# Kernel optimization log

Measured on AMD Instinct MI355X. Metric: run time of the kernel, lower is better.

Reference implementation:

```python
import jax, jax.numpy as jnp
import numpy as np

SCALE = 100.0
ALPHA_MEM = 0.9
ALPHA_MEM_OUT = 0.9
ALPHA_R = 0.85
ALPHA_X = 0.95
ALPHA_P = 0.95
ALPHA_D = 0.95
WMIN = 0.0
WMAX = 2.0


@jax.custom_vjp
def spike_fn(x):
    # SurrGradSpike.forward: heaviside(x)
    return (x > 0).astype(x.dtype)

def _spike_fwd(x):
    return spike_fn(x), x

def _spike_bwd(x, g):
    # SurrGradSpike.backward: g / (scale*|x| + 1)^2
    return (g / (SCALE * jnp.abs(x) + 1.0) ** 2,)

spike_fn.defvjp(_spike_fwd, _spike_bwd)


def setup_inputs() -> dict:
    key = jax.random.key(0)
    ks = jax.random.split(key, 8)
    B, T, NI, N, NO, D = 8, 64, 256, 512, 32, 4
    inputs = jax.random.normal(ks[0], (B, T, NI), jnp.float32)
    w = jax.random.normal(ks[1], (N, N), jnp.float32) * (0.1 / np.sqrt(N))
    w_in = jax.random.normal(ks[2], (NI, N), jnp.float32) * (1.0 / np.sqrt(NI))
    w_out = jax.random.normal(ks[3], (N, NO), jnp.float32) * (1.0 / np.sqrt(N))
    # each synapse (e,o) assigned exactly one delay bin -> one-hot delay map (D,N,N)
    delay_idx = jax.random.randint(ks[4], (N, N), 0, D)
    dmap = jax.nn.one_hot(delay_idx, D, axis=0, dtype=jnp.float32)
    delays = jnp.array([1, 2, 3, 5], jnp.int32)
    w_signs = jnp.where(jnp.arange(N) < (4 * N) // 5, 1.0, -1.0).astype(jnp.float32)
    p = jax.random.uniform(ks[5], (N,), jnp.float32, minval=-0.5, maxval=0.5)
    A_p = jax.random.uniform(ks[6], (N, N), jnp.float32, minval=0.0, maxval=1e-3)
    A_d = jax.random.uniform(ks[7], (N, N), jnp.float32, minval=0.0, maxval=1e-3)
    return dict(inputs=inputs, w=w, w_in=w_in, w_out=w_out, dmap=dmap,
                delays=delays, w_signs=w_signs, p=p, A_p=A_p, A_d=A_d)


def _snn_forward(inputs, w, w_in, w_out, dmap, delays, w_signs, p, A_p, A_d):
    B, T, _ = inputs.shape
    N = w.shape[0]
    dt = inputs.dtype
    # epoch state
    inp = jnp.einsum('btc,cn->btn', inputs, w_in)          # (B,T,N)
    W = dmap * (w_signs[:, None] * jnp.abs(w))             # (D,N,N)
    p_depr = (p < 0).astype(dt)

    mem = jnp.zeros((B, N), dt)
    w_p = jnp.zeros((B, N), dt)
    x_bar = jnp.zeros((B, N), dt)
    u_pot = jnp.zeros((B, N), dt)
    u_dep = jnp.zeros((B, N), dt)
    w_stdp = jnp.ones((B, N, N), dt)
    rec_out = jnp.zeros((T, B, N), dt)
    rec_wp = jnp.zeros((T, B, N), dt)
    rec_xb = jnp.zeros((T, B, N), dt)

    def step(carry, xt):
        mem, w_p, x_bar, u_pot, u_dep, w_stdp, rec_out, rec_wp, rec_xb = carry
        t, inp_t = xt
        # mark_spikes + record_state (records pre-update values)
        spike = spike_fn(mem - 1.0)
        rec_out = rec_out.at[t].set(spike)
        rec_wp = rec_wp.at[t].set(w_p)
        rec_xb = rec_xb.at[t].set(x_bar)
        # delayed gathers; negative torch indices hit zero-initialized tail -> %T
        idx = (t - delays) % T
        out_del = jnp.take(rec_out, idx, axis=0)           # (D,B,N)
        wp_del = jnp.take(rec_wp, idx, axis=0)
        xb_del = jnp.take(rec_xb, idx, axis=0)
        # synaptic input
        syn_p = out_del * (1.0 + wp_del)
        syn = jnp.einsum('dbe,deo,beo->bo', syn_p, W, w_stdp)
        # STP
        dw_p = spike * p * (1.0 + p_depr * w_p)
        w_p = w_p * ALPHA_R + dw_p
        # STDP (uses pre-update u_dep/u_pot/mem)
        X = jnp.einsum('dbe,deo->beo', out_del, dmap)
        dW_dep = X * A_d[None] * jax.nn.relu(u_dep)[:, None, :]
        xbar_d = jnp.einsum('dbe,deo->beo', xb_del, dmap)
        dW_pot = xbar_d * A_p[None] * (jax.lax.stop_gradient(spike) * jax.nn.relu(u_pot))[:, None, :]
        x_bar = ALPHA_X * x_bar + (1.0 - ALPHA_X) * jax.lax.stop_gradient(spike)
        u_pot = ALPHA_P * u_pot + (1.0 - ALPHA_P) * mem
        u_dep = ALPHA_D * u_dep + (1.0 - ALPHA_D) * mem
        w_stdp = jnp.clip(w_stdp + dW_pot - dW_dep, WMIN, WMAX)
        # membrane integration with spike reset (detached)
        mem = ALPHA_MEM * mem + inp_t + syn - jax.lax.stop_gradient(spike)
        return (mem, w_p, x_bar, u_pot, u_dep, w_stdp, rec_out, rec_wp, rec_xb), None

    carry = (mem, w_p, x_bar, u_pot, u_dep, w_stdp, rec_out, rec_wp, rec_xb)
    xs = (jnp.arange(T), jnp.swapaxes(inp, 0, 1))
    carry, _ = jax.lax.scan(jax.checkpoint(step), carry, xs)
    rec_out = carry[6]                                     # (T,B,N)
    # readout: leaky integrator over projected spikes
    h2 = jnp.einsum('btn,no->bto', jnp.swapaxes(rec_out, 0, 1), w_out)

    def ro_step(o, h):
        o = ALPHA_MEM_OUT * o + h
        return o, o

    _, readout = jax.lax.scan(ro_step, jnp.zeros((B, h2.shape[-1]), dt),
                              jnp.swapaxes(h2, 0, 1))
    return jnp.swapaxes(readout, 0, 1)                     # (B,T,n_outputs)


def reference(inputs, w, w_in, w_out, dmap, delays, w_signs, p, A_p, A_d):
    return _snn_forward(inputs, w, w_in, w_out, dmap, delays, w_signs, p, A_p, A_d)
```

## Files before the change

### kernel.cpp

```cpp
#include <hip/hip_runtime.h>
#include <stdint.h>


#define B  8
#define T  64
#define NI 256
#define NN 512
#define NO 32
#define DD 4

#define NBLK 256
#define TPB  512
#define OPB  16
#define EGR  32
#define SPL  16
#define EPAD 516

#define REC_ELEMS (T*B*NN)
#define MAGIC  0x534E4E31u

#define C_CNT   0
#define C_GCNT  8
#define C_PAR   9
#define C_HDR   10
#define C_DONE  16

__device__ __forceinline__ unsigned long long rec_load(const unsigned long long* p) {
    return __hip_atomic_load(p, __ATOMIC_RELAXED, __HIP_MEMORY_SCOPE_AGENT);
}
__device__ __forceinline__ unsigned long long rec_load_plain(const unsigned long long* p) {
    return *p;
}
__device__ __forceinline__ void rec_store(unsigned long long* p, unsigned long long v) {
    __hip_atomic_store(p, v, __ATOMIC_RELAXED, __HIP_MEMORY_SCOPE_AGENT);
}
__device__ __forceinline__ unsigned ctrl_ld(const unsigned* p) {
    return __hip_atomic_load(p, __ATOMIC_RELAXED, __HIP_MEMORY_SCOPE_AGENT);
}
__device__ __forceinline__ void ctrl_st(unsigned* p, unsigned v) {
    __hip_atomic_store(p, v, __ATOMIC_RELAXED, __HIP_MEMORY_SCOPE_AGENT);
}
__device__ __forceinline__ bool unwritten(unsigned long long v, unsigned runpar) {
    return ((unsigned)v >> 31) != runpar;
}
__device__ __forceinline__ unsigned long long poll_written(
        const unsigned long long* src, unsigned long long v, unsigned runpar) {
    int guard = 0;
    while (unwritten(v, runpar)) {
        if (guard >= 2) __builtin_amdgcn_s_sleep(1);
        v = rec_load(src);
        if (++guard > (1 << 18)) break;
    }
    return v;
}

#define BAR_LDS() do {                                      \
    asm volatile("s_waitcnt lgkmcnt(0)" ::: "memory");      \
    __builtin_amdgcn_s_barrier();                           \
    asm volatile("" ::: "memory");                          \
} while (0)

__global__ __launch_bounds__(TPB, 2)
void snn_main(const float* __restrict__ inputs,
              const float* __restrict__ w,
              const float* __restrict__ w_in,
              const float* __restrict__ w_out,
              const float* __restrict__ dmap,
              const int*   __restrict__ delays,
              const float* __restrict__ w_signs,
              const float* __restrict__ p,
              const float* __restrict__ A_p,
              const float* __restrict__ A_d,
              unsigned long long* __restrict__ rec,
              float* __restrict__ h2buf,
              unsigned* __restrict__ ctrl,
              float* __restrict__ out)
{
    __shared__ float2 sxq[DD*EPAD];
    __shared__ float  inp_s[T*OPB];
    __shared__ float  red[8*OPB];
    __shared__ unsigned int spikebits_s[T];
    __shared__ float  wout16_s[OPB*NO];
    __shared__ float  h2_s[T*NO];
    __shared__ int    last_s;

    const int tid     = threadIdx.x;
    const int bid     = blockIdx.x;
    const int b       = bid & 7;
    const int chunk   = bid >> 3;
    const int o_base  = chunk * OPB;
    const int o_local = tid & 15;
    const int e_grp   = tid >> 4;
    const int o       = o_base + o_local;

    unsigned runpar;
    if (ctrl_ld(ctrl + C_HDR) != MAGIC) {
        {
            unsigned long long* base = rec + (size_t)bid * (REC_ELEMS / NBLK);
            #pragma unroll
            for (int i = 0; i < REC_ELEMS / NBLK / TPB; ++i)
                rec_store(base + i*TPB + tid, 0x0000000080000000ull);
        }
        {
            unsigned* hb = (unsigned*)h2buf + (size_t)bid * ((B*T*NO) / NBLK);
            if (tid < (B*T*NO) / NBLK) ctrl_st(hb + tid, 0u);
        }
        if (bid == 0 && tid < 10) ctrl_st(ctrl + tid, 0u);
        __syncthreads();
        if (tid == 0) ctrl_st(ctrl + C_DONE + bid, MAGIC);
        if (tid < NBLK) {
            int guard = 0;
            while (ctrl_ld(ctrl + C_DONE + tid) != MAGIC) {
                __builtin_amdgcn_s_sleep(2);
                if (++guard > (1 << 20)) break;
            }
        }
        __syncthreads();
        runpar = 0u;
    } else {
        runpar = ctrl_ld(ctrl + C_PAR);
    }

    if (tid < OPB) {
        rec_store(rec + (size_t)(0*B + b)*NN + o_base + tid,
                  (unsigned long long)(runpar << 31));
    }
    if (tid == 0) spikebits_s[0] = 0u;

    float wv[SPL], ap[SPL], ad[SPL], ws[SPL];
    int   laddr[SPL];
    #pragma unroll
    for (int i = 0; i < SPL; ++i) {
        const int e = e_grp + EGR*i;
        wv[i] = w_signs[e] * fabsf(w[e*NN + o]);
        ap[i] = A_p[e*NN + o];
        ad[i] = A_d[e*NN + o];
        int d = 0;
        if (dmap[1*NN*NN + e*NN + o] != 0.0f) d = 1;
        if (dmap[2*NN*NN + e*NN + o] != 0.0f) d = 2;
        if (dmap[3*NN*NN + e*NN + o] != 0.0f) d = 3;
        ws[i]    = 1.0f;
        laddr[i] = (d*EPAD + e) * 8;
    }
    int del[DD];
    #pragma unroll
    for (int d = 0; d < DD; ++d) del[d] = delays[d];

    {
        float* win = (float*)sxq;
        #pragma unroll
        for (int q = 0; q < NI*OPB/TPB; ++q) {
            const int k = q*TPB + tid;
            const int c = k >> 4, oo = k & 15;
            win[c*OPB + oo] = w_in[c*NN + o_base + oo];
        }
        __syncthreads();
        #pragma unroll
        for (int j = 0; j < T/EGR; ++j) {
            const int tj = e_grp*(T/EGR) + j;
            const float* inrow = inputs + (size_t)(b*T + tj)*NI;
            float a = 0.f;
            for (int c = 0; c < NI; ++c) a += inrow[c] * win[c*OPB + o_local];
            inp_s[tj*OPB + o_local] = a;
        }
        __syncthreads();
    }

    #pragma unroll
    for (int d = 0; d < DD; ++d)
        sxq[d*EPAD + tid] = make_float2(0.f, 0.f);
    __syncthreads();

    float mem = 0.f, w_p = 0.f, x_bar = 0.f, u_pot = 0.f, u_dep = 0.f;
    const float p_o  = p[o];
    const float pd_o = (p_o < 0.f) ? 1.f : 0.f;

    unsigned long long pf[DD];
    const int stage_ord[DD] = {1, 2, 3, 0};

    for (int t = 0; t < T; ++t) {
        if (t + 1 < T) {
            #pragma unroll
            for (int d = 0; d < DD; ++d) {
                if (t + 1 >= del[d]) {
                    const int s = (t + 1 - del[d]) & 63;
                    const unsigned long long* src = rec + (size_t)(s*B + b)*NN + tid;
                    pf[d] = (del[d] == 1) ? rec_load(src) : rec_load_plain(src);
                }
            }
        }

        const float spike = (mem > 1.0f) ? 1.0f : 0.0f;
        const float pg  = spike * fmaxf(u_pot, 0.f);
        const float udr = fmaxf(u_dep, 0.f);
        float2 v[SPL];
        float acc = 0.f;
        #pragma unroll
        for (int i = 0; i < SPL; ++i) {
            v[i] = *(const float2*)((const char*)sxq + laddr[i]);
            acc = fmaf(v[i].x, wv[i]*ws[i], acc);
        }
        float a2 = acc + __shfl_xor(acc, 16);
        a2 += __shfl_xor(a2, 32);
        if ((tid & 63) < 16) red[(tid >> 6)*16 + o_local] = a2;
        BAR_LDS();
        float syn = 0.f;
        #pragma unroll
        for (int k = 0; k < 8; ++k) syn += red[k*16 + o_local];

        const float wp_new = 0.85f*w_p + spike * p_o * (1.f + pd_o*w_p);
        const float xb_new = 0.95f*x_bar + 0.05f*spike;
        u_pot = 0.95f*u_pot + 0.05f*mem;
        u_dep = 0.95f*u_dep + 0.05f*mem;
        mem   = 0.9f*mem + inp_s[t*OPB + o_local] + syn - spike;
        w_p   = wp_new;
        x_bar = xb_new;

        if (t + 1 < T && tid < OPB) {
            const float spike1 = (mem > 1.0f) ? 1.0f : 0.0f;
            const float sp = spike1 * (1.f + w_p);
            const unsigned int xu = __float_as_uint(x_bar) | (spike1 != 0.f ? 0x80000000u : 0u);
            const unsigned int lo = __float_as_uint(sp) | (runpar << 31);
            const unsigned long long pk = ((unsigned long long)xu << 32) | lo;
            rec_store(rec + (size_t)((t+1)*B + b)*NN + o_base + tid, pk);
            const unsigned long long bal = __ballot(spike1 != 0.0f);
            if (tid == 0) spikebits_s[t+1] = (unsigned int)bal;
        }

        #pragma unroll
        for (int i = 0; i < SPL; ++i) {
            const unsigned int xu = __float_as_uint(v[i].y);
            const float dep = ((int)xu < 0) ? ad[i]*udr : 0.f;
            const float pot = (ap[i]*pg) * fabsf(v[i].y);
            ws[i] = fminf(fmaxf(ws[i] + pot - dep, 0.f), 2.f);
        }

        if (t + 1 < T) {
            #pragma unroll
            for (int j = 0; j < DD; ++j) {
                const int d = stage_ord[j];
                unsigned long long v0 = (unsigned long long)(runpar << 31);
                if (t + 1 >= del[d]) {
                    const int s = (t + 1 - del[d]) & 63;
                    const unsigned long long* src = rec + (size_t)(s*B + b)*NN + tid;
                    v0 = poll_written(src, pf[d], runpar);
                }
                sxq[d*EPAD + tid] =
                    make_float2(__uint_as_float((unsigned)v0 & 0x7fffffffu),
                                __uint_as_float((unsigned)(v0 >> 32)));
            }
        }
        BAR_LDS();
    }

    if (tid < OPB*NO) wout16_s[tid] = w_out[(o_base + (tid >> 5))*NO + (tid & 31)];
    __syncthreads();

    const int g  = tid >> 5;
    const int oo = tid & 31;
    #pragma unroll
    for (int j = 0; j < 4; ++j) {
        const int t = g*4 + j;
        const unsigned int bits = spikebits_s[t];
        float a = 0.f;
        #pragma unroll
        for (int i = 0; i < OPB; ++i)
            if (bits & (1u << i)) a += wout16_s[i*NO + oo];
        if (a != 0.f) atomicAdd(h2buf + ((size_t)b*T + t)*NO + oo, a);
    }
    __threadfence();
    __syncthreads();
    if (tid == 0) last_s = (atomicAdd(ctrl + C_CNT + b, 1u) == 31u) ? 1 : 0;
    __syncthreads();

    if (last_s) {
        __threadfence();
        #pragma unroll
        for (int j = 0; j < 4; ++j) {
            const int t = g*4 + j;
            h2_s[t*NO + oo] = __hip_atomic_load(h2buf + ((size_t)b*T + t)*NO + oo,
                                                __ATOMIC_RELAXED, __HIP_MEMORY_SCOPE_AGENT);
        }
        __syncthreads();
        if (tid < NO) {
            float st = 0.f;
            for (int t = 0; t < T; ++t) {
                st = 0.9f*st + h2_s[t*NO + tid];
                out[((size_t)b*T + t)*NO + tid] = st;
            }
        }
    }

    if (tid == 0) {
        const unsigned gar = __hip_atomic_fetch_add(ctrl + C_GCNT, 1u,
                                                    __ATOMIC_ACQ_REL, __HIP_MEMORY_SCOPE_AGENT);
        if (gar == NBLK - 1) {
            for (int i = 0; i < 8; ++i) ctrl_st(ctrl + C_CNT + i, 0u);
            ctrl_st(ctrl + C_GCNT, 0u);
            ctrl_st(ctrl + C_PAR, runpar ^ 1u);
            ctrl_st(ctrl + C_HDR, MAGIC);
        }
    }
}

extern "C" void kernel_launch(void* const* d_in, const int* in_sizes, int n_in,
                              void* d_out, int out_size, void* d_ws, size_t ws_size,
                              hipStream_t stream)
{
    const float* inputs  = (const float*)d_in[0];
    const float* w       = (const float*)d_in[1];
    const float* w_in    = (const float*)d_in[2];
    const float* w_out   = (const float*)d_in[3];
    const float* dmap    = (const float*)d_in[4];
    const int*   delays  = (const int*)  d_in[5];
    const float* w_signs = (const float*)d_in[6];
    const float* p       = (const float*)d_in[7];
    const float* A_p     = (const float*)d_in[8];
    const float* A_d     = (const float*)d_in[9];

    char* wsb = (char*)d_ws;
    unsigned long long* rec = (unsigned long long*)wsb;
    float* h2buf = (float*)(wsb + (size_t)REC_ELEMS*8);
    unsigned* ctrl = (unsigned*)(wsb + (size_t)REC_ELEMS*8 + (size_t)B*T*NO*4);

    hipLaunchKernelGGL(snn_main, dim3(NBLK), dim3(TPB), 0, stream,
                       inputs, w, w_in, w_out, dmap, delays, w_signs, p, A_p, A_d,
                       rec, h2buf, ctrl, (float*)d_out);
}
```

Before: 223.3 us.

## Double-buffer delay staging with 1024 threads per block to halve per-step barriers

Block size grows from 512 to 1024 threads, so each thread handles 8 presynaptic rows instead of 16. The two thread halves each stage two of the four delay buffers. Staging of the next step's spike records now goes into a second LDS buffer and overlaps the current step's matvec, so one barrier per timestep is removed. This also changes initialisation indexing and zeroes h2buf in the last block. It risks higher register pressure and a larger cross-half reduction, and the cooperative spin-wait now depends on more resident threads.

```diff
diff --git a/kernel.cpp b/kernel.cpp
--- a/kernel.cpp
+++ b/kernel.cpp
@@ -10,10 +10,10 @@
 #define DD 4
 
 #define NBLK 256
-#define TPB  512
+#define TPB  1024
 #define OPB  16
-#define EGR  32
-#define SPL  16
+#define EGR  64
+#define SPL  8
 #define EPAD 516
 
 #define REC_ELEMS (T*B*NN)
@@ -60,7 +60,7 @@
     asm volatile("" ::: "memory");                          \
 } while (0)
 
-__global__ __launch_bounds__(TPB, 2)
+__global__ __launch_bounds__(TPB, 4)
 void snn_main(const float* __restrict__ inputs,
               const float* __restrict__ w,
               const float* __restrict__ w_in,
@@ -76,9 +76,9 @@
               unsigned* __restrict__ ctrl,
               float* __restrict__ out)
 {
-    __shared__ float2 sxq[DD*EPAD];
+    __shared__ float2 sxq[2][DD*EPAD];
     __shared__ float  inp_s[T*OPB];
-    __shared__ float  red[8*OPB];
+    __shared__ float  red[2][16*OPB];
     __shared__ unsigned int spikebits_s[T];
     __shared__ float  wout16_s[OPB*NO];
     __shared__ float  h2_s[T*NO];
@@ -92,19 +92,15 @@
     const int o_local = tid & 15;
     const int e_grp   = tid >> 4;
     const int o       = o_base + o_local;
+    const int slotid  = tid & 511;
+    const int hi      = tid >> 9;
 
     unsigned runpar;
     if (ctrl_ld(ctrl + C_HDR) != MAGIC) {
-        {
-            unsigned long long* base = rec + (size_t)bid * (REC_ELEMS / NBLK);
-            #pragma unroll
-            for (int i = 0; i < REC_ELEMS / NBLK / TPB; ++i)
-                rec_store(base + i*TPB + tid, 0x0000000080000000ull);
-        }
-        {
-            unsigned* hb = (unsigned*)h2buf + (size_t)bid * ((B*T*NO) / NBLK);
-            if (tid < (B*T*NO) / NBLK) ctrl_st(hb + tid, 0u);
-        }
+        rec_store(rec + (size_t)bid * (REC_ELEMS / NBLK) + tid,
+                  0x0000000080000000ull);
+        if (tid < (B*T*NO) / NBLK)
+            ctrl_st((unsigned*)h2buf + (size_t)bid * ((B*T*NO) / NBLK) + tid, 0u);
         if (bid == 0 && tid < 10) ctrl_st(ctrl + tid, 0u);
         __syncthreads();
         if (tid == 0) ctrl_st(ctrl + C_DONE + bid, MAGIC);
@@ -145,6 +141,8 @@
     int del[DD];
     #pragma unroll
     for (int d = 0; d < DD; ++d) del[d] = delays[d];
+    const int dj0 = hi ? 2 : 1;
+    const int dj1 = hi ? 0 : 3;
 
     {
         float* win = (float*)sxq;
@@ -155,38 +153,42 @@
             win[c*OPB + oo] = w_in[c*NN + o_base + oo];
         }
         __syncthreads();
-        #pragma unroll
-        for (int j = 0; j < T/EGR; ++j) {
-            const int tj = e_grp*(T/EGR) + j;
+        {
+            const int tj = tid >> 4;
             const float* inrow = inputs + (size_t)(b*T + tj)*NI;
             float a = 0.f;
             for (int c = 0; c < NI; ++c) a += inrow[c] * win[c*OPB + o_local];
+            __syncthreads();
             inp_s[tj*OPB + o_local] = a;
         }
-        __syncthreads();
-    }
-
-    #pragma unroll
-    for (int d = 0; d < DD; ++d)
-        sxq[d*EPAD + tid] = make_float2(0.f, 0.f);
+    }
+
+    if (tid < 512) {
+        #pragma unroll
+        for (int d = 0; d < DD; ++d)
+            sxq[0][d*EPAD + tid] = make_float2(0.f, 0.f);
+    }
     __syncthreads();
 
     float mem = 0.f, w_p = 0.f, x_bar = 0.f, u_pot = 0.f, u_dep = 0.f;
     const float p_o  = p[o];
     const float pd_o = (p_o < 0.f) ? 1.f : 0.f;
 
-    unsigned long long pf[DD];
-    const int stage_ord[DD] = {1, 2, 3, 0};
-
     for (int t = 0; t < T; ++t) {
+        const int cur = t & 1, nxt = cur ^ 1;
+        const char* sxc = (const char*)&sxq[cur][0];
+
+        unsigned long long pf0 = 0ull, pf1 = 0ull;
         if (t + 1 < T) {
-            #pragma unroll
-            for (int d = 0; d < DD; ++d) {
-                if (t + 1 >= del[d]) {
-                    const int s = (t + 1 - del[d]) & 63;
-                    const unsigned long long* src = rec + (size_t)(s*B + b)*NN + tid;
-                    pf[d] = (del[d] == 1) ? rec_load(src) : rec_load_plain(src);
-                }
+            if (t + 1 >= del[dj0]) {
+                const int s = (t + 1 - del[dj0]) & 63;
+                const unsigned long long* src = rec + (size_t)(s*B + b)*NN + slotid;
+                pf0 = (del[dj0] == 1) ? rec_load(src) : rec_load_plain(src);
+            }
+            if (t + 1 >= del[dj1]) {
+                const int s = (t + 1 - del[dj1]) & 63;
+                const unsigned long long* src = rec + (size_t)(s*B + b)*NN + slotid;
+                pf1 = (del[dj1] == 1) ? rec_load(src) : rec_load_plain(src);
             }
         }
 
@@ -197,16 +199,41 @@
         float acc = 0.f;
         #pragma unroll
         for (int i = 0; i < SPL; ++i) {
-            v[i] = *(const float2*)((const char*)sxq + laddr[i]);
+            v[i] = *(const float2*)(sxc + laddr[i]);
             acc = fmaf(v[i].x, wv[i]*ws[i], acc);
         }
         float a2 = acc + __shfl_xor(acc, 16);
         a2 += __shfl_xor(a2, 32);
-        if ((tid & 63) < 16) red[(tid >> 6)*16 + o_local] = a2;
+        if ((tid & 63) < 16) red[cur][(tid >> 6)*16 + o_local] = a2;
+
+        if (t + 1 < T) {
+            {
+                unsigned long long v0 = (unsigned long long)(runpar << 31);
+                if (t + 1 >= del[dj0]) {
+                    const int s = (t + 1 - del[dj0]) & 63;
+                    v0 = poll_written(rec + (size_t)(s*B + b)*NN + slotid, pf0, runpar);
+                }
+                sxq[nxt][dj0*EPAD + slotid] =
+                    make_float2(__uint_as_float((unsigned)v0 & 0x7fffffffu),
+                                __uint_as_float((unsigned)(v0 >> 32)));
+            }
+            {
+                unsigned long long v1 = (unsigned long long)(runpar << 31);
+                if (t + 1 >= del[dj1]) {
+                    const int s = (t + 1 - del[dj1]) & 63;
+                    v1 = poll_written(rec + (size_t)(s*B + b)*NN + slotid, pf1, runpar);
+                }
+                sxq[nxt][dj1*EPAD + slotid] =
+                    make_float2(__uint_as_float((unsigned)v1 & 0x7fffffffu),
+                                __uint_as_float((unsigned)(v1 >> 32)));
+            }
+        }
+
         BAR_LDS();
+
         float syn = 0.f;
         #pragma unroll
-        for (int k = 0; k < 8; ++k) syn += red[k*16 + o_local];
+        for (int k = 0; k < 16; ++k) syn += red[cur][k*16 + o_local];
 
         const float wp_new = 0.85f*w_p + spike * p_o * (1.f + pd_o*w_p);
         const float xb_new = 0.95f*x_bar + 0.05f*spike;
@@ -234,33 +261,17 @@
             const float pot = (ap[i]*pg) * fabsf(v[i].y);
             ws[i] = fminf(fmaxf(ws[i] + pot - dep, 0.f), 2.f);
         }
-
-        if (t + 1 < T) {
-            #pragma unroll
-            for (int j = 0; j < DD; ++j) {
-                const int d = stage_ord[j];
-                unsigned long long v0 = (unsigned long long)(runpar << 31);
-                if (t + 1 >= del[d]) {
-                    const int s = (t + 1 - del[d]) & 63;
-                    const unsigned long long* src = rec + (size_t)(s*B + b)*NN + tid;
-                    v0 = poll_written(src, pf[d], runpar);
-                }
-                sxq[d*EPAD + tid] =
-                    make_float2(__uint_as_float((unsigned)v0 & 0x7fffffffu),
-                                __uint_as_float((unsigned)(v0 >> 32)));
-            }
-        }
-        BAR_LDS();
-    }
-
+    }
+
+    __syncthreads();
     if (tid < OPB*NO) wout16_s[tid] = w_out[(o_base + (tid >> 5))*NO + (tid & 31)];
     __syncthreads();
 
     const int g  = tid >> 5;
     const int oo = tid & 31;
     #pragma unroll
-    for (int j = 0; j < 4; ++j) {
-        const int t = g*4 + j;
+    for (int j = 0; j < 2; ++j) {
+        const int t = g*2 + j;
         const unsigned int bits = spikebits_s[t];
         float a = 0.f;
         #pragma unroll
@@ -276,12 +287,18 @@
     if (last_s) {
         __threadfence();
         #pragma unroll
-        for (int j = 0; j < 4; ++j) {
-            const int t = g*4 + j;
+        for (int j = 0; j < 2; ++j) {
+            const int t = g*2 + j;
             h2_s[t*NO + oo] = __hip_atomic_load(h2buf + ((size_t)b*T + t)*NO + oo,
                                                 __ATOMIC_RELAXED, __HIP_MEMORY_SCOPE_AGENT);
         }
         __syncthreads();
+        #pragma unroll
+        for (int j = 0; j < 2; ++j) {
+            const int t = g*2 + j;
+            __hip_atomic_store((unsigned*)(h2buf + ((size_t)b*T + t)*NO + oo), 0u,
+                               __ATOMIC_RELAXED, __HIP_MEMORY_SCOPE_AGENT);
+        }
         if (tid < NO) {
             float st = 0.f;
             for (int t = 0; t < T; ++t) {
```

Measured after the change: 249.1 us. 11.5% more time.

## Load delayed spikes directly from global per synapse, drop LDS staging barrier

Applied to the files above, without the earlier changes.

Replaces the per-step LDS staging of delayed presynaptic state (with polling and a second block barrier) by having each thread prefetch its 16 synapse values straight from the global recurrence buffer, indexed by a precomputed per-synapse delay offset. Values for the next step are double-buffered in registers and only polled if the parity bit shows they are unwritten, and the reduction buffer is double-buffered so one barrier per step suffices. This removes a barrier and LDS traffic per timestep, at the cost of 16 uncoalesced global atomic loads per thread per step instead of 4 coalesced ones. It also reuses shared scratch and zeroes h2buf in the last block so the next call starts clean.

```diff
diff --git a/kernel.cpp b/kernel.cpp
--- a/kernel.cpp
+++ b/kernel.cpp
@@ -14,8 +14,8 @@
 #define OPB  16
 #define EGR  32
 #define SPL  16
-#define EPAD 516
-
+
+#define RECB (B*NN*8)
 #define REC_ELEMS (T*B*NN)
 #define MAGIC  0x534E4E31u
 
@@ -28,9 +28,6 @@
 __device__ __forceinline__ unsigned long long rec_load(const unsigned long long* p) {
     return __hip_atomic_load(p, __ATOMIC_RELAXED, __HIP_MEMORY_SCOPE_AGENT);
 }
-__device__ __forceinline__ unsigned long long rec_load_plain(const unsigned long long* p) {
-    return *p;
-}
 __device__ __forceinline__ void rec_store(unsigned long long* p, unsigned long long v) {
     __hip_atomic_store(p, v, __ATOMIC_RELAXED, __HIP_MEMORY_SCOPE_AGENT);
 }
@@ -42,16 +39,6 @@
 }
 __device__ __forceinline__ bool unwritten(unsigned long long v, unsigned runpar) {
     return ((unsigned)v >> 31) != runpar;
-}
-__device__ __forceinline__ unsigned long long poll_written(
-        const unsigned long long* src, unsigned long long v, unsigned runpar) {
-    int guard = 0;
-    while (unwritten(v, runpar)) {
-        if (guard >= 2) __builtin_amdgcn_s_sleep(1);
-        v = rec_load(src);
-        if (++guard > (1 << 18)) break;
-    }
-    return v;
 }
 
 #define BAR_LDS() do {                                      \
@@ -76,12 +63,10 @@
               unsigned* __restrict__ ctrl,
               float* __restrict__ out)
 {
-    __shared__ float2 sxq[DD*EPAD];
+    __shared__ float scratch[NI*OPB];
     __shared__ float  inp_s[T*OPB];
-    __shared__ float  red[8*OPB];
+    __shared__ float  red[2][8*OPB];
     __shared__ unsigned int spikebits_s[T];
-    __shared__ float  wout16_s[OPB*NO];
-    __shared__ float  h2_s[T*NO];
     __shared__ int    last_s;
 
     const int tid     = threadIdx.x;
@@ -101,10 +86,8 @@
             for (int i = 0; i < REC_ELEMS / NBLK / TPB; ++i)
                 rec_store(base + i*TPB + tid, 0x0000000080000000ull);
         }
-        {
-            unsigned* hb = (unsigned*)h2buf + (size_t)bid * ((B*T*NO) / NBLK);
-            if (tid < (B*T*NO) / NBLK) ctrl_st(hb + tid, 0u);
-        }
+        if (tid < (B*T*NO) / NBLK)
+            ctrl_st((unsigned*)h2buf + (size_t)bid * ((B*T*NO) / NBLK) + tid, 0u);
         if (bid == 0 && tid < 10) ctrl_st(ctrl + tid, 0u);
         __syncthreads();
         if (tid == 0) ctrl_st(ctrl + C_DONE + bid, MAGIC);
@@ -128,7 +111,8 @@
     if (tid == 0) spikebits_s[0] = 0u;
 
     float wv[SPL], ap[SPL], ad[SPL], ws[SPL];
-    int   laddr[SPL];
+    int   voff[SPL];
+    unsigned long long dpk = 0ull;
     #pragma unroll
     for (int i = 0; i < SPL; ++i) {
         const int e = e_grp + EGR*i;
@@ -139,18 +123,15 @@
         if (dmap[1*NN*NN + e*NN + o] != 0.0f) d = 1;
         if (dmap[2*NN*NN + e*NN + o] != 0.0f) d = 2;
         if (dmap[3*NN*NN + e*NN + o] != 0.0f) d = 3;
-        ws[i]    = 1.0f;
-        laddr[i] = (d*EPAD + e) * 8;
-    }
-    int del[DD];
-    #pragma unroll
-    for (int d = 0; d < DD; ++d) del[d] = delays[d];
+        const int dly = delays[d];
+        ws[i]   = 1.0f;
+        dpk    |= (unsigned long long)(unsigned)dly << (4*i);
+        voff[i] = (b*NN + e)*8 - dly*RECB;
+    }
 
     {
-        float* win = (float*)sxq;
-        #pragma unroll
-        for (int q = 0; q < NI*OPB/TPB; ++q) {
-            const int k = q*TPB + tid;
+        float* win = scratch;
+        for (int k = tid; k < NI*OPB; k += TPB) {
             const int c = k >> 4, oo = k & 15;
             win[c*OPB + oo] = w_in[c*NN + o_base + oo];
         }
@@ -166,26 +147,39 @@
         __syncthreads();
     }
 
-    #pragma unroll
-    for (int d = 0; d < DD; ++d)
-        sxq[d*EPAD + tid] = make_float2(0.f, 0.f);
-    __syncthreads();
-
     float mem = 0.f, w_p = 0.f, x_bar = 0.f, u_pot = 0.f, u_dep = 0.f;
     const float p_o  = p[o];
     const float pd_o = (p_o < 0.f) ? 1.f : 0.f;
 
-    unsigned long long pf[DD];
-    const int stage_ord[DD] = {1, 2, 3, 0};
-
-    for (int t = 0; t < T; ++t) {
+    const float tz = __uint_as_float(runpar << 31);
+    float2 vA[SPL], vB[SPL];
+    #pragma unroll
+    for (int i = 0; i < SPL; ++i) vA[i] = make_float2(tz, 0.f);
+
+    auto STEP = [&](int t, float2 (&vc)[SPL], float2 (&vn)[SPL]) {
+        const char* base1 = (const char*)rec + (size_t)(t+1)*RECB;
+
         if (t + 1 < T) {
-            #pragma unroll
-            for (int d = 0; d < DD; ++d) {
-                if (t + 1 >= del[d]) {
-                    const int s = (t + 1 - del[d]) & 63;
-                    const unsigned long long* src = rec + (size_t)(s*B + b)*NN + tid;
-                    pf[d] = (del[d] == 1) ? rec_load(src) : rec_load_plain(src);
+            if (t >= 4) {
+                #pragma unroll
+                for (int i = 0; i < SPL; ++i) {
+                    const unsigned long long v =
+                        rec_load((const unsigned long long*)(base1 + (long)voff[i]));
+                    vn[i] = make_float2(__uint_as_float((unsigned)v),
+                                        __uint_as_float((unsigned)(v >> 32)));
+                }
+            } else {
+                #pragma unroll
+                for (int i = 0; i < SPL; ++i) {
+                    const int dly = (int)((dpk >> (4*i)) & 15ull);
+                    float2 r = make_float2(tz, 0.f);
+                    if (t + 1 >= dly) {
+                        const unsigned long long v =
+                            rec_load((const unsigned long long*)(base1 + (long)voff[i]));
+                        r = make_float2(__uint_as_float((unsigned)v),
+                                        __uint_as_float((unsigned)(v >> 32)));
+                    }
+                    vn[i] = r;
                 }
             }
         }
@@ -193,20 +187,33 @@
         const float spike = (mem > 1.0f) ? 1.0f : 0.0f;
         const float pg  = spike * fmaxf(u_pot, 0.f);
         const float udr = fmaxf(u_dep, 0.f);
-        float2 v[SPL];
         float acc = 0.f;
         #pragma unroll
         for (int i = 0; i < SPL; ++i) {
-            v[i] = *(const float2*)((const char*)sxq + laddr[i]);
-            acc = fmaf(v[i].x, wv[i]*ws[i], acc);
-        }
+            unsigned lo = __float_as_uint(vc[i].x);
+            if (__builtin_expect((lo >> 31) != runpar, 0)) {
+                const unsigned long long* srcf = (const unsigned long long*)
+                    ((const char*)rec + (size_t)t*RECB + (long)voff[i]);
+                unsigned long long v; int guard = 0;
+                do {
+                    v = rec_load(srcf);
+                    if (++guard > 2) __builtin_amdgcn_s_sleep(1);
+                    if (guard > (1 << 18)) break;
+                } while (unwritten(v, runpar));
+                lo = (unsigned)v;
+                vc[i].y = __uint_as_float((unsigned)(v >> 32));
+            }
+            const float x = __uint_as_float(lo & 0x7fffffffu);
+            acc = fmaf(x, wv[i]*ws[i], acc);
+        }
+
         float a2 = acc + __shfl_xor(acc, 16);
         a2 += __shfl_xor(a2, 32);
-        if ((tid & 63) < 16) red[(tid >> 6)*16 + o_local] = a2;
+        if ((tid & 63) < 16) red[t & 1][(tid >> 6)*16 + o_local] = a2;
         BAR_LDS();
         float syn = 0.f;
         #pragma unroll
-        for (int k = 0; k < 8; ++k) syn += red[k*16 + o_local];
+        for (int k = 0; k < 8; ++k) syn += red[t & 1][k*16 + o_local];
 
         const float wp_new = 0.85f*w_p + spike * p_o * (1.f + pd_o*w_p);
         const float xb_new = 0.95f*x_bar + 0.05f*spike;
@@ -229,31 +236,23 @@
 
         #pragma unroll
         for (int i = 0; i < SPL; ++i) {
-            const unsigned int xu = __float_as_uint(v[i].y);
+            const unsigned int xu = __float_as_uint(vc[i].y);
             const float dep = ((int)xu < 0) ? ad[i]*udr : 0.f;
-            const float pot = (ap[i]*pg) * fabsf(v[i].y);
+            const float pot = (ap[i]*pg) * fabsf(vc[i].y);
             ws[i] = fminf(fmaxf(ws[i] + pot - dep, 0.f), 2.f);
         }
-
-        if (t + 1 < T) {
-            #pragma unroll
-            for (int j = 0; j < DD; ++j) {
-                const int d = stage_ord[j];
-                unsigned long long v0 = (unsigned long long)(runpar << 31);
-                if (t + 1 >= del[d]) {
-                    const int s = (t + 1 - del[d]) & 63;
-                    const unsigned long long* src = rec + (size_t)(s*B + b)*NN + tid;
-                    v0 = poll_written(src, pf[d], runpar);
-                }
-                sxq[d*EPAD + tid] =
-                    make_float2(__uint_as_float((unsigned)v0 & 0x7fffffffu),
-                                __uint_as_float((unsigned)(v0 >> 32)));
-            }
-        }
-        BAR_LDS();
-    }
-
-    if (tid < OPB*NO) wout16_s[tid] = w_out[(o_base + (tid >> 5))*NO + (tid & 31)];
+    };
+
+    for (int t = 0; t < T; t += 2) {
+        STEP(t,     vA, vB);
+        STEP(t + 1, vB, vA);
+    }
+
+    __syncthreads();
+    float* wout16_s = scratch;
+    float* h2_s     = scratch + OPB*NO;
+    for (int k = tid; k < OPB*NO; k += TPB)
+        wout16_s[k] = w_out[(o_base + (k >> 5))*NO + (k & 31)];
     __syncthreads();
 
     const int g  = tid >> 5;
@@ -282,6 +281,12 @@
                                                 __ATOMIC_RELAXED, __HIP_MEMORY_SCOPE_AGENT);
         }
         __syncthreads();
+        #pragma unroll
+        for (int j = 0; j < 4; ++j) {
+            const int t = g*4 + j;
+            __hip_atomic_store((unsigned*)(h2buf + ((size_t)b*T + t)*NO + oo), 0u,
+                               __ATOMIC_RELAXED, __HIP_MEMORY_SCOPE_AGENT);
+        }
         if (tid < NO) {
             float st = 0.f;
             for (int t = 0; t < T; ++t) {
```

Result: slower. 412.7 us (+84.8%).

## Use half as many blocks with 32 outputs each and fuse STDP update

Applied to the files above, without the earlier changes.

Each block now handles 32 output neurons instead of 16, so the persistent grid drops from 256 to 128 blocks and each thread processes 32 presynaptic synapses. The input projection is staged in two halves of w_in so it fits in the shared buffer. The per-synapse STDP weight update is folded into the synaptic accumulation loop, which removes the float2 register array and one shuffle stage. The aim is to cut the number of blocks taking part in the per-timestep cross-block handoff and the polling traffic that goes with it. The cost is a longer serial inner loop per thread and more registers for the per-synapse state.

```diff
diff --git a/kernel.cpp b/kernel.cpp
--- a/kernel.cpp
+++ b/kernel.cpp
@@ -9,11 +9,11 @@
 #define NO 32
 #define DD 4
 
-#define NBLK 256
+#define NBLK 128
 #define TPB  512
-#define OPB  16
-#define EGR  32
-#define SPL  16
+#define OPB  32
+#define EGR  16
+#define SPL  32
 #define EPAD 516
 
 #define REC_ELEMS (T*B*NN)
@@ -80,7 +80,7 @@
     __shared__ float  inp_s[T*OPB];
     __shared__ float  red[8*OPB];
     __shared__ unsigned int spikebits_s[T];
-    __shared__ float  wout16_s[OPB*NO];
+    __shared__ float  wout_s[OPB*NO];
     __shared__ float  h2_s[T*NO];
     __shared__ int    last_s;
 
@@ -89,8 +89,8 @@
     const int b       = bid & 7;
     const int chunk   = bid >> 3;
     const int o_base  = chunk * OPB;
-    const int o_local = tid & 15;
-    const int e_grp   = tid >> 4;
+    const int o_local = tid & 31;
+    const int e_grp   = tid >> 5;
     const int o       = o_base + o_local;
 
     unsigned runpar;
@@ -148,21 +148,32 @@
 
     {
         float* win = (float*)sxq;
-        #pragma unroll
-        for (int q = 0; q < NI*OPB/TPB; ++q) {
-            const int k = q*TPB + tid;
-            const int c = k >> 4, oo = k & 15;
-            win[c*OPB + oo] = w_in[c*NN + o_base + oo];
-        }
-        __syncthreads();
-        #pragma unroll
-        for (int j = 0; j < T/EGR; ++j) {
-            const int tj = e_grp*(T/EGR) + j;
-            const float* inrow = inputs + (size_t)(b*T + tj)*NI;
-            float a = 0.f;
-            for (int c = 0; c < NI; ++c) a += inrow[c] * win[c*OPB + o_local];
-            inp_s[tj*OPB + o_local] = a;
-        }
+        float a[T/EGR];
+        #pragma unroll
+        for (int j = 0; j < T/EGR; ++j) a[j] = 0.f;
+        #pragma unroll
+        for (int half = 0; half < 2; ++half) {
+            const int c0 = half * (NI/2);
+            #pragma unroll
+            for (int q = 0; q < (NI/2)*OPB/TPB; ++q) {
+                const int k = q*TPB + tid;
+                const int c = k >> 5, oo = k & 31;
+                win[c*OPB + oo] = w_in[(c0 + c)*NN + o_base + oo];
+            }
+            __syncthreads();
+            #pragma unroll
+            for (int j = 0; j < T/EGR; ++j) {
+                const int tj = e_grp*(T/EGR) + j;
+                const float* inrow = inputs + (size_t)(b*T + tj)*NI + c0;
+                float s = 0.f;
+                for (int c = 0; c < NI/2; ++c) s += inrow[c] * win[c*OPB + o_local];
+                a[j] += s;
+            }
+            __syncthreads();
+        }
+        #pragma unroll
+        for (int j = 0; j < T/EGR; ++j)
+            inp_s[(e_grp*(T/EGR) + j)*OPB + o_local] = a[j];
         __syncthreads();
     }
 
@@ -193,20 +204,22 @@
         const float spike = (mem > 1.0f) ? 1.0f : 0.0f;
         const float pg  = spike * fmaxf(u_pot, 0.f);
         const float udr = fmaxf(u_dep, 0.f);
-        float2 v[SPL];
         float acc = 0.f;
         #pragma unroll
         for (int i = 0; i < SPL; ++i) {
-            v[i] = *(const float2*)((const char*)sxq + laddr[i]);
-            acc = fmaf(v[i].x, wv[i]*ws[i], acc);
-        }
-        float a2 = acc + __shfl_xor(acc, 16);
-        a2 += __shfl_xor(a2, 32);
-        if ((tid & 63) < 16) red[(tid >> 6)*16 + o_local] = a2;
+            const float2 v = *(const float2*)((const char*)sxq + laddr[i]);
+            acc = fmaf(v.x, wv[i]*ws[i], acc);
+            const unsigned int xu = __float_as_uint(v.y);
+            const float dep = ((int)xu < 0) ? ad[i]*udr : 0.f;
+            const float pot = (ap[i]*pg) * fabsf(v.y);
+            ws[i] = fminf(fmaxf(ws[i] + pot - dep, 0.f), 2.f);
+        }
+        const float a2 = acc + __shfl_xor(acc, 32);
+        if ((tid & 63) < 32) red[(tid >> 6)*32 + o_local] = a2;
         BAR_LDS();
         float syn = 0.f;
         #pragma unroll
-        for (int k = 0; k < 8; ++k) syn += red[k*16 + o_local];
+        for (int k = 0; k < 8; ++k) syn += red[k*32 + o_local];
 
         const float wp_new = 0.85f*w_p + spike * p_o * (1.f + pd_o*w_p);
         const float xb_new = 0.95f*x_bar + 0.05f*spike;
@@ -225,14 +238,6 @@
             rec_store(rec + (size_t)((t+1)*B + b)*NN + o_base + tid, pk);
             const unsigned long long bal = __ballot(spike1 != 0.0f);
             if (tid == 0) spikebits_s[t+1] = (unsigned int)bal;
-        }
-
-        #pragma unroll
-        for (int i = 0; i < SPL; ++i) {
-            const unsigned int xu = __float_as_uint(v[i].y);
-            const float dep = ((int)xu < 0) ? ad[i]*udr : 0.f;
-            const float pot = (ap[i]*pg) * fabsf(v[i].y);
-            ws[i] = fminf(fmaxf(ws[i] + pot - dep, 0.f), 2.f);
         }
 
         if (t + 1 < T) {
@@ -253,7 +258,8 @@
         BAR_LDS();
     }
 
-    if (tid < OPB*NO) wout16_s[tid] = w_out[(o_base + (tid >> 5))*NO + (tid & 31)];
+    for (int k = tid; k < OPB*NO; k += TPB)
+        wout_s[k] = w_out[(o_base + (k >> 5))*NO + (k & 31)];
     __syncthreads();
 
     const int g  = tid >> 5;
@@ -265,12 +271,12 @@
         float a = 0.f;
         #pragma unroll
         for (int i = 0; i < OPB; ++i)
-            if (bits & (1u << i)) a += wout16_s[i*NO + oo];
+            if (bits & (1u << i)) a += wout_s[i*NO + oo];
         if (a != 0.f) atomicAdd(h2buf + ((size_t)b*T + t)*NO + oo, a);
     }
     __threadfence();
     __syncthreads();
-    if (tid == 0) last_s = (atomicAdd(ctrl + C_CNT + b, 1u) == 31u) ? 1 : 0;
+    if (tid == 0) last_s = (atomicAdd(ctrl + C_CNT + b, 1u) == (NBLK/B - 1)) ? 1 : 0;
     __syncthreads();
 
     if (last_s) {
```

After: 275.1 us. 23.2% more time.
